# Performance work log

Hardware: AMD Instinct MI355X
Metric: run time of the kernel (lower is better)

Reference implementation:

```python
import jax, jax.numpy as jnp
import numpy as np

D_MODEL = 1024
H = 16
D_K = D_MODEL // H
B, S = 2, 2048
NEG = -1e9


def setup_inputs() -> dict:
    key = jax.random.key(0)
    ks = jax.random.split(key, 8)
    scale = 1.0 / np.sqrt(D_MODEL)
    q = jax.random.normal(ks[0], (B, S, D_MODEL), dtype=jnp.float32)
    k = jax.random.normal(ks[1], (B, S, D_MODEL), dtype=jnp.float32)
    v = jax.random.normal(ks[2], (B, S, D_MODEL), dtype=jnp.float32)
    # causal 0/1 mask, broadcastable to [B, h, S, S]
    mask = jnp.tril(jnp.ones((S, S), dtype=jnp.int32))[None, None, :, :]
    w_q = jax.random.normal(ks[3], (D_MODEL, D_MODEL), dtype=jnp.float32) * scale
    w_k = jax.random.normal(ks[4], (D_MODEL, D_MODEL), dtype=jnp.float32) * scale
    w_v = jax.random.normal(ks[5], (D_MODEL, D_MODEL), dtype=jnp.float32) * scale
    w_o = jax.random.normal(ks[6], (D_MODEL, D_MODEL), dtype=jnp.float32) * scale
    return {"q": q, "k": k, "v": v, "mask": mask,
            "w_q": w_q, "w_k": w_k, "w_v": w_v, "w_o": w_o}


def reference(q, k, v, mask, w_q, w_k, w_v, w_o):
    # projections (no bias)
    def split_heads(x):
        Bn, Sn, _ = x.shape
        return x.reshape(Bn, Sn, H, D_K).transpose(0, 2, 1, 3)  # [B,h,S,d_k]

    qh = split_heads(q @ w_q)
    kh = split_heads(k @ w_k)
    vh = split_heads(v @ w_v)

    scores = jnp.einsum('bhqd,bhkd->bhqk', qh, kh) / jnp.sqrt(
        jnp.asarray(D_K, dtype=qh.dtype))
    scores = jnp.where(mask == 0, jnp.asarray(NEG, dtype=scores.dtype), scores)
    attn = jax.nn.softmax(scores, axis=-1)  # dropout rate 0.0 -> identity
    x = jnp.einsum('bhqk,bhkd->bhqd', attn, vh)  # [B,h,S,d_k]
    x = x.transpose(0, 2, 1, 3).reshape(q.shape[0], q.shape[1], D_MODEL)
    return x @ w_o
```

## Files before the change

### kernel.cpp

```cpp
#include <hip/hip_runtime.h>

#define D_MODEL 1024
#define NH 16
#define DK 64
#define BB 2
#define SS 2048
#define M_TOT (BB*SS)

typedef float f32x4 __attribute__((ext_vector_type(4)));
typedef float f32x16 __attribute__((ext_vector_type(16)));
typedef __bf16 bf16x8 __attribute__((ext_vector_type(8)));
typedef unsigned int u32;

#define QSCALE 0.1803368801f
#define DEFER_THR 11.5416f

__device__ __forceinline__ unsigned short f2bf(float f){
  unsigned int u = __float_as_uint(f);
  unsigned int r = (u + 0x7fffu + ((u >> 16) & 1u)) >> 16;
  return (unsigned short)r;
}

__device__ __forceinline__ void gload_lds16(const void* g, void* l){
  __builtin_amdgcn_global_load_lds((const __attribute__((address_space(1))) void*)g,
                                   (__attribute__((address_space(3))) void*)l,
                                   16, 0, 0);
}

__device__ __forceinline__ void swap_half(u32 a, u32 b, int hi, u32& x, u32& y){
#if __has_builtin(__builtin_amdgcn_permlane32_swap)
  typedef unsigned int uint2v __attribute__((ext_vector_type(2)));
  uint2v r = __builtin_amdgcn_permlane32_swap(a, b, false, false);
  x = r.x; y = r.y;
#else
  u32 as = __shfl_xor(a, 32);
  u32 bs = __shfl_xor(b, 32);
  x = hi ? bs : a;
  y = hi ? b  : as;
#endif
}

__global__ __launch_bounds__(256) void transpose_cvt4(const float* __restrict__ wq,
                                                      const float* __restrict__ wk,
                                                      const float* __restrict__ wv,
                                                      const float* __restrict__ wo,
                                                      unsigned short* __restrict__ WqkvT,
                                                      unsigned short* __restrict__ woT){
  __shared__ float tile[64][65];
  const int which = blockIdx.z;
  const float* w = (which == 0) ? wq : (which == 1) ? wk : (which == 2) ? wv : wo;
  unsigned short* wt = (which == 3) ? woT : (WqkvT + (size_t)which * 1024 * 1024);
  const int N = D_MODEL;
  const int bx = blockIdx.x * 64;
  const int by = blockIdx.y * 64;
  const int t = threadIdx.x;
  #pragma unroll
  for (int i = 0; i < 16; ++i){
    int idx = t + i * 256;
    int r = idx >> 6, c = idx & 63;
    tile[r][c] = w[(size_t)(by + r) * N + bx + c];
  }
  __syncthreads();
  #pragma unroll
  for (int i = 0; i < 16; ++i){
    int idx = t + i * 256;
    int r = idx >> 6, c = idx & 63;
    wt[(size_t)(bx + r) * N + by + c] = f2bf(tile[c][r]);
  }
}

__global__ __launch_bounds__(256) void gemm_qkv(const float* __restrict__ Aq,
                                                const float* __restrict__ Ak,
                                                const float* __restrict__ Av,
                                                const unsigned short* __restrict__ WT,
                                                unsigned short* __restrict__ Qh,
                                                unsigned short* __restrict__ Kh,
                                                unsigned short* __restrict__ VhT){
  __shared__ float          Af[2][128 * 32];
  __shared__ unsigned short Bl[2][128 * 32];
  const int tid = threadIdx.x;
  const int wid = tid >> 6, lane = tid & 63;
  const int lr = lane & 15, lg = lane >> 4;
  const int wm = wid >> 1, wn = wid & 1;
  const int bm = blockIdx.x, bn = blockIdx.y;
  const int seg = bn >> 3;
  const float* A = (seg == 0) ? Aq : (seg == 1) ? Ak : Av;
  const int K = D_MODEL;

  f32x4 acc[4][4];
  #pragma unroll
  for (int i = 0; i < 4; ++i)
    #pragma unroll
    for (int j = 0; j < 4; ++j)
      acc[i][j] = (f32x4){0.f, 0.f, 0.f, 0.f};

  const int lr8 = lane >> 3;
  const int lc8 = lane & 7;
  const int ls8 = lc8 ^ lr8;

  auto stage = [&](int buf, int kt){
    #pragma unroll
    for (int i = 0; i < 4; ++i){
      const int g = wid * 4 + i;
      const int r = g * 8 + lr8;
      gload_lds16(A + (size_t)(bm * 128 + r) * K + kt * 32 + ls8 * 4,
                  &Af[buf][g * 256]);
    }
    #pragma unroll
    for (int rr = 0; rr < 2; ++rr){
      int vt = tid + rr * 256;
      int row = vt >> 2, c8 = (vt & 3) * 8;
      gload_lds16(WT + (size_t)(bn * 128 + row) * K + kt * 32 + c8,
                  &Bl[buf][(wid << 9) + rr * 2048]);
    }
  };

  stage(0, 0);
  int cur = 0;
  for (int kt = 0; kt < 32; ++kt){
    __syncthreads();
    if (kt + 1 < 32) stage(cur ^ 1, kt + 1);
    bf16x8 af[4], bfr[4];
    const int rs = lr & 7;
    #pragma unroll
    for (int i = 0; i < 4; ++i){
      const int row = wm * 64 + i * 16 + lr;
      f32x4 a0 = *(const f32x4*)&Af[cur][row * 32 + (((2 * lg)     ^ rs) * 4)];
      f32x4 a1 = *(const f32x4*)&Af[cur][row * 32 + (((2 * lg + 1) ^ rs) * 4)];
      u32 cc[4];
      asm("v_cvt_pk_bf16_f32 %0, %1, %2" : "=v"(cc[0]) : "v"(a0[0]), "v"(a0[1]));
      asm("v_cvt_pk_bf16_f32 %0, %1, %2" : "=v"(cc[1]) : "v"(a0[2]), "v"(a0[3]));
      asm("v_cvt_pk_bf16_f32 %0, %1, %2" : "=v"(cc[2]) : "v"(a1[0]), "v"(a1[1]));
      asm("v_cvt_pk_bf16_f32 %0, %1, %2" : "=v"(cc[3]) : "v"(a1[2]), "v"(a1[3]));
      __builtin_memcpy(&af[i], cc, 16);
    }
    #pragma unroll
    for (int j = 0; j < 4; ++j)
      bfr[j] = *(const bf16x8*)&Bl[cur][(wn * 64 + j * 16 + lr) * 32 + lg * 8];
    #pragma unroll
    for (int i = 0; i < 4; ++i)
      #pragma unroll
      for (int j = 0; j < 4; ++j)
        acc[i][j] = __builtin_amdgcn_mfma_f32_16x16x32_bf16(af[i], bfr[j], acc[i][j], 0, 0, 0);
    cur ^= 1;
  }

  if (seg < 2){
    unsigned short* O = (seg == 0) ? Qh : Kh;
    const float sc = (seg == 0) ? QSCALE : 1.0f;
    #pragma unroll
    for (int i = 0; i < 4; ++i){
      int row0 = bm * 128 + wm * 64 + i * 16 + lg * 4;
      #pragma unroll
      for (int j = 0; j < 4; ++j){
        int colseg = (bn & 7) * 128 + wn * 64 + j * 16 + lr;
        int h = colseg >> 6, dk = colseg & 63;
        #pragma unroll
        for (int p = 0; p < 4; ++p){
          int rowm = row0 + p;
          int b = rowm >> 11, s = rowm & 2047;
          O[((size_t)(b * NH + h) * SS + s) * DK + dk] = f2bf(acc[i][j][p] * sc);
        }
      }
    }
  } else {
    #pragma unroll
    for (int i = 0; i < 4; ++i){
      int row0 = bm * 128 + wm * 64 + i * 16 + lg * 4;
      int b = row0 >> 11, s = row0 & 2047;
      #pragma unroll
      for (int j = 0; j < 4; ++j){
        int colseg = (bn & 7) * 128 + wn * 64 + j * 16 + lr;
        int h = colseg >> 6, dk = colseg & 63;
        ushort4 o4;
        o4.x = f2bf(acc[i][j][0]); o4.y = f2bf(acc[i][j][1]);
        o4.z = f2bf(acc[i][j][2]); o4.w = f2bf(acc[i][j][3]);
        *(ushort4*)&VhT[((size_t)(b * NH + h) * DK + dk) * SS + s] = o4;
      }
    }
  }
}

__global__ __launch_bounds__(256) void gemm_o64(const unsigned short* __restrict__ A,
                                                const unsigned short* __restrict__ Bt,
                                                float* __restrict__ O){
  __shared__ unsigned short Al[2][64 * 32];
  __shared__ unsigned short Bl[2][128 * 32];
  const int tid = threadIdx.x;
  const int wid = tid >> 6, lane = tid & 63;
  const int lr = lane & 15, lg = lane >> 4;
  const int wm = wid >> 1, wn = wid & 1;
  const int bm = blockIdx.x, bn = blockIdx.y;
  const int K = D_MODEL;

  f32x4 acc[2][4];
  #pragma unroll
  for (int i = 0; i < 2; ++i)
    #pragma unroll
    for (int j = 0; j < 4; ++j)
      acc[i][j] = (f32x4){0.f, 0.f, 0.f, 0.f};

  auto stage = [&](int buf, int kt){
    {
      int row = tid >> 2, c8 = (tid & 3) * 8;
      gload_lds16(A + (size_t)(bm * 64 + row) * K + kt * 32 + c8,
                  &Al[buf][wid << 9]);
    }
    #pragma unroll
    for (int r = 0; r < 2; ++r){
      int vt = tid + r * 256;
      int row = vt >> 2, c8 = (vt & 3) * 8;
      gload_lds16(Bt + (size_t)(bn * 128 + row) * K + kt * 32 + c8,
                  &Bl[buf][(wid << 9) + r * 2048]);
    }
  };

  stage(0, 0);
  int cur = 0;
  for (int kt = 0; kt < 32; ++kt){
    __syncthreads();
    if (kt + 1 < 32) stage(cur ^ 1, kt + 1);
    bf16x8 af[2], bfr[4];
    #pragma unroll
    for (int i = 0; i < 2; ++i)
      af[i] = *(const bf16x8*)&Al[cur][(wm * 32 + i * 16 + lr) * 32 + lg * 8];
    #pragma unroll
    for (int j = 0; j < 4; ++j)
      bfr[j] = *(const bf16x8*)&Bl[cur][(wn * 64 + j * 16 + lr) * 32 + lg * 8];
    #pragma unroll
    for (int i = 0; i < 2; ++i)
      #pragma unroll
      for (int j = 0; j < 4; ++j)
        acc[i][j] = __builtin_amdgcn_mfma_f32_16x16x32_bf16(af[i], bfr[j], acc[i][j], 0, 0, 0);
    cur ^= 1;
  }

  #pragma unroll
  for (int i = 0; i < 2; ++i){
    int row0 = bm * 64 + wm * 32 + i * 16 + lg * 4;
    #pragma unroll
    for (int j = 0; j < 4; ++j){
      int col = bn * 128 + wn * 64 + j * 16 + lr;
      #pragma unroll
      for (int p = 0; p < 4; ++p)
        O[(size_t)(row0 + p) * D_MODEL + col] = acc[i][j][p];
    }
  }
}

__global__ __launch_bounds__(256) void attn_kernel(const unsigned short* __restrict__ Qh,
                                                   const unsigned short* __restrict__ Kh,
                                                   const unsigned short* __restrict__ VhT,
                                                   unsigned short* __restrict__ Oc){
  __shared__ unsigned short SL[2][4][4096];
  const int bh = blockIdx.x;
  const int px = blockIdx.y;
  const int tid = threadIdx.x, wid = tid >> 6, lane = tid & 63;
  const int ln = lane & 31, hi = lane >> 5;
  const int qh = wid & 1, pp = wid >> 1;
  const int b = bh >> 4, h = bh & 15;
  const size_t kvbase = (size_t)bh * SS * DK;

  #pragma unroll 1
  for (int segq = 0; segq < 2; ++segq){
    const int qblk = segq ? (31 - px) : px;
    const int q0 = qblk * 64 + qh * 32;
    const int Tw = 2 * qblk + qh;
    const int R = (qblk + 2) >> 1;

    const unsigned short* qp = Qh + kvbase + (size_t)(q0 + ln) * DK + hi * 8;
    bf16x8 qbv[4];
    #pragma unroll
    for (int c = 0; c < 4; ++c) qbv[c] = *(const bf16x8*)(qp + c * 16);

    f32x16 oa0 = {0,0,0,0,0,0,0,0,0,0,0,0,0,0,0,0};
    f32x16 oa1 = {0,0,0,0,0,0,0,0,0,0,0,0,0,0,0,0};
    float m = -1e30f, ls = 0.f;

    auto stage = [&](int bufb, int r){
      const int k0A = (2 * r) * 64;
      const int k0B = k0A + 64;
      const bool haveB = (2 * r + 1) <= qblk;
      #pragma unroll
      for (int i = 0; i < 2; ++i){
        const int c = i * 256 + tid;
        const int row = c >> 3;
        const int slot = (c & 7) ^ (row & 7);
        const int ldso = (i * 256 + wid * 64) * 8;
        gload_lds16(Kh  + kvbase + (size_t)(k0A + row) * DK + slot * 8, &SL[bufb][0][ldso]);
        gload_lds16(VhT + kvbase + (size_t)row * SS + k0A + slot * 8,   &SL[bufb][1][ldso]);
        if (haveB){
          gload_lds16(Kh  + kvbase + (size_t)(k0B + row) * DK + slot * 8, &SL[bufb][2][ldso]);
          gload_lds16(VhT + kvbase + (size_t)row * SS + k0B + slot * 8,   &SL[bufb][3][ldso]);
        }
      }
    };

    stage(0, 0);
    int cur = 0;
    #pragma unroll 1
    for (int r = 0; r < R; ++r){
      __syncthreads();
      if (r + 1 < R) stage(cur ^ 1, r + 1);

      const int t = 2 * r + pp;
      if (t <= qblk){
        const unsigned short* Kb = SL[cur][pp * 2];
        const unsigned short* Vb = SL[cur][pp * 2 + 1];

        f32x16 sta = {0,0,0,0,0,0,0,0,0,0,0,0,0,0,0,0};
        f32x16 stb = {0,0,0,0,0,0,0,0,0,0,0,0,0,0,0,0};
        __builtin_amdgcn_s_setprio(1);
        #pragma unroll
        for (int c = 0; c < 4; ++c){
          const int po = ((c * 2 + hi) ^ (ln & 7)) * 8;
          bf16x8 kfa = *(const bf16x8*)&Kb[ln * 64 + po];
          bf16x8 kfb = *(const bf16x8*)&Kb[(32 + ln) * 64 + po];
          sta = __builtin_amdgcn_mfma_f32_32x32x16_bf16(kfa, qbv[c], sta, 0, 0, 0);
          stb = __builtin_amdgcn_mfma_f32_32x32x16_bf16(kfb, qbv[c], stb, 0, 0, 0);
        }
        __builtin_amdgcn_s_setprio(0);

        const int ta = 2 * t, tb = 2 * t + 1;
        if (tb == Tw){
          #pragma unroll
          for (int rr = 0; rr < 16; ++rr){
            int kg = (rr & 3) + 8 * (rr >> 2) + 4 * hi;
            if (kg > ln) stb[rr] = -1e30f;
          }
        } else if (ta == Tw){
          #pragma unroll
          for (int rr = 0; rr < 16; ++rr){
            int kg = (rr & 3) + 8 * (rr >> 2) + 4 * hi;
            if (kg > ln) sta[rr] = -1e30f;
            stb[rr] = -1e30f;
          }
        }

        float tm[8];
        #pragma unroll
        for (int i = 0; i < 8; ++i)
          tm[i] = fmaxf(fmaxf(sta[2*i], sta[2*i+1]), fmaxf(stb[2*i], stb[2*i+1]));
        float mx = fmaxf(fmaxf(fmaxf(tm[0], tm[1]), fmaxf(tm[2], tm[3])),
                         fmaxf(fmaxf(tm[4], tm[5]), fmaxf(tm[6], tm[7])));
        mx = fmaxf(mx, __shfl_xor(mx, 32));

        if (__any(mx > m + DEFER_THR)){
          const float mn = fmaxf(m, mx);
          const float fac = __builtin_amdgcn_exp2f(m - mn);
          m = mn;
          ls *= fac;
          #pragma unroll
          for (int rr = 0; rr < 16; ++rr){ oa0[rr] *= fac; oa1[rr] *= fac; }
        }

        #pragma unroll
        for (int rr = 0; rr < 16; ++rr){
          sta[rr] = __builtin_amdgcn_exp2f(sta[rr] - m);
          stb[rr] = __builtin_amdgcn_exp2f(stb[rr] - m);
        }
        float sm[8];
        #pragma unroll
        for (int i = 0; i < 8; ++i)
          sm[i] = (sta[2*i] + sta[2*i+1]) + (stb[2*i] + stb[2*i+1]);
        float rsum = ((sm[0] + sm[1]) + (sm[2] + sm[3])) + ((sm[4] + sm[5]) + (sm[6] + sm[7]));
        rsum += __shfl_xor(rsum, 32);
        ls += rsum;

        u32 ca[8], cb[8];
        #pragma unroll
        for (int i = 0; i < 8; ++i){
          asm("v_cvt_pk_bf16_f32 %0, %1, %2" : "=v"(ca[i]) : "v"(sta[2*i]), "v"(sta[2*i+1]));
          asm("v_cvt_pk_bf16_f32 %0, %1, %2" : "=v"(cb[i]) : "v"(stb[2*i]), "v"(stb[2*i+1]));
        }
        u32 w0[4], w1[4], w2[4], w3[4];
        swap_half(ca[0], ca[2], hi, w0[0], w0[2]);
        swap_half(ca[1], ca[3], hi, w0[1], w0[3]);
        swap_half(ca[4], ca[6], hi, w1[0], w1[2]);
        swap_half(ca[5], ca[7], hi, w1[1], w1[3]);
        swap_half(cb[0], cb[2], hi, w2[0], w2[2]);
        swap_half(cb[1], cb[3], hi, w2[1], w2[3]);
        swap_half(cb[4], cb[6], hi, w3[0], w3[2]);
        swap_half(cb[5], cb[7], hi, w3[1], w3[3]);
        bf16x8 pf[4];
        __builtin_memcpy(&pf[0], w0, 16);
        __builtin_memcpy(&pf[1], w1, 16);
        __builtin_memcpy(&pf[2], w2, 16);
        __builtin_memcpy(&pf[3], w3, 16);

        __builtin_amdgcn_s_setprio(1);
        #pragma unroll
        for (int ks = 0; ks < 4; ++ks){
          const int po = ((ks * 2 + hi) ^ (ln & 7)) * 8;
          bf16x8 v0 = *(const bf16x8*)&Vb[ln * 64 + po];
          bf16x8 v1 = *(const bf16x8*)&Vb[(32 + ln) * 64 + po];
          oa0 = __builtin_amdgcn_mfma_f32_32x32x16_bf16(v0, pf[ks], oa0, 0, 0, 0);
          oa1 = __builtin_amdgcn_mfma_f32_32x32x16_bf16(v1, pf[ks], oa1, 0, 0, 0);
        }
        __builtin_amdgcn_s_setprio(0);
      }
      cur ^= 1;
    }
    __syncthreads();

    float* oL  = (float*)&SL[0][0][0];
    float* mLs = (float*)&SL[0][2][0];
    if (wid >= 2){
      const int w = wid - 2;
      #pragma unroll
      for (int rr = 0; rr < 16; ++rr){
        oL[(w * 32 + rr) * 64 + lane]      = oa0[rr];
        oL[(w * 32 + 16 + rr) * 64 + lane] = oa1[rr];
      }
      if (hi == 0){ mLs[w * 32 + ln] = m; mLs[64 + w * 32 + ln] = ls; }
    }
    __syncthreads();
    if (wid < 2){
      const float m1  = mLs[wid * 32 + ln];
      const float ls1 = mLs[64 + wid * 32 + ln];
      const float mstar = fmaxf(m, m1);
      const float f0 = __builtin_amdgcn_exp2f(m  - mstar);
      const float f1 = __builtin_amdgcn_exp2f(m1 - mstar);
      const float inv = 1.0f / (f0 * ls + f1 * ls1);
      const size_t rowbase = ((size_t)b * SS + q0 + ln) * D_MODEL + h * DK;
      #pragma unroll
      for (int g = 0; g < 4; ++g){
        ushort4 o4;
        o4.x = f2bf((f0 * oa0[4*g + 0] + f1 * oL[(wid * 32 + 4*g + 0) * 64 + lane]) * inv);
        o4.y = f2bf((f0 * oa0[4*g + 1] + f1 * oL[(wid * 32 + 4*g + 1) * 64 + lane]) * inv);
        o4.z = f2bf((f0 * oa0[4*g + 2] + f1 * oL[(wid * 32 + 4*g + 2) * 64 + lane]) * inv);
        o4.w = f2bf((f0 * oa0[4*g + 3] + f1 * oL[(wid * 32 + 4*g + 3) * 64 + lane]) * inv);
        *(ushort4*)&Oc[rowbase + 8*g + 4*hi] = o4;
      }
      #pragma unroll
      for (int g = 0; g < 4; ++g){
        ushort4 o4;
        o4.x = f2bf((f0 * oa1[4*g + 0] + f1 * oL[(wid * 32 + 16 + 4*g + 0) * 64 + lane]) * inv);
        o4.y = f2bf((f0 * oa1[4*g + 1] + f1 * oL[(wid * 32 + 16 + 4*g + 1) * 64 + lane]) * inv);
        o4.z = f2bf((f0 * oa1[4*g + 2] + f1 * oL[(wid * 32 + 16 + 4*g + 2) * 64 + lane]) * inv);
        o4.w = f2bf((f0 * oa1[4*g + 3] + f1 * oL[(wid * 32 + 16 + 4*g + 3) * 64 + lane]) * inv);
        *(ushort4*)&Oc[rowbase + 32 + 8*g + 4*hi] = o4;
      }
    }
    __syncthreads();
  }
}

extern "C" void kernel_launch(void* const* d_in, const int* in_sizes, int n_in,
                              void* d_out, int out_size, void* d_ws, size_t ws_size,
                              hipStream_t stream){
  const float* q  = (const float*)d_in[0];
  const float* k  = (const float*)d_in[1];
  const float* v  = (const float*)d_in[2];
  const float* wq = (const float*)d_in[4];
  const float* wk = (const float*)d_in[5];
  const float* wv = (const float*)d_in[6];
  const float* wo = (const float*)d_in[7];
  float* out = (float*)d_out;

  char* ws = (char*)d_ws;
  const size_t MB = 1024 * 1024;
  unsigned short* WqkvT  = (unsigned short*)(ws + 0 * MB);
  unsigned short* woT    = (unsigned short*)(ws + 6 * MB);
  unsigned short* Qh     = (unsigned short*)(ws + 8 * MB);
  unsigned short* Kh     = (unsigned short*)(ws + 16 * MB);
  unsigned short* VhT    = (unsigned short*)(ws + 24 * MB);
  unsigned short* attnb  = (unsigned short*)(ws + 32 * MB);

  dim3 tg(16, 16, 4);
  transpose_cvt4<<<tg, 256, 0, stream>>>(wq, wk, wv, wo, WqkvT, woT);

  dim3 gqkv(M_TOT / 128, 3 * D_MODEL / 128);
  gemm_qkv<<<gqkv, 256, 0, stream>>>(q, k, v, WqkvT, Qh, Kh, VhT);

  dim3 ga(BB * NH, SS / 128);
  attn_kernel<<<ga, 256, 0, stream>>>(Qh, Kh, VhT, attnb);

  dim3 go(M_TOT / 64, D_MODEL / 128);
  gemm_o64<<<go, 256, 0, stream>>>(attnb, woT, out);
}
```

Before: 118.7 us.

## Convert QKV GEMM A tile to bf16 in registers before LDS store

The QKV projection GEMM used to stream fp32 activations straight into LDS with direct global-to-LDS loads, then convert to bf16 on every fragment read. It now loads the fp32 A tile into registers, converts once to bf16, and writes it to a bf16 LDS buffer after the MFMA block. This halves LDS footprint and read traffic for A and avoids converting the same data repeatedly across warps. In exchange it loses the async direct-to-LDS path, adds register pressure, and drops the XOR swizzle, which may bring LDS bank conflicts.

```diff
diff --git a/kernel.cpp b/kernel.cpp
--- a/kernel.cpp
+++ b/kernel.cpp
@@ -76,7 +76,7 @@
                                                 unsigned short* __restrict__ Qh,
                                                 unsigned short* __restrict__ Kh,
                                                 unsigned short* __restrict__ VhT){
-  __shared__ float          Af[2][128 * 32];
+  __shared__ unsigned short Al[2][128 * 32];
   __shared__ unsigned short Bl[2][128 * 32];
   const int tid = threadIdx.x;
   const int wid = tid >> 6, lane = tid & 63;
@@ -94,18 +94,27 @@
     for (int j = 0; j < 4; ++j)
       acc[i][j] = (f32x4){0.f, 0.f, 0.f, 0.f};
 
-  const int lr8 = lane >> 3;
-  const int lc8 = lane & 7;
-  const int ls8 = lc8 ^ lr8;
-
-  auto stage = [&](int buf, int kt){
-    #pragma unroll
-    for (int i = 0; i < 4; ++i){
-      const int g = wid * 4 + i;
-      const int r = g * 8 + lr8;
-      gload_lds16(A + (size_t)(bm * 128 + r) * K + kt * 32 + ls8 * 4,
-                  &Af[buf][g * 256]);
-    }
+  const int arow  = tid >> 3;
+  const int aslot = tid & 7;
+
+  f32x4 ar[4];
+
+  auto loadA = [&](int kt){
+    #pragma unroll
+    for (int p = 0; p < 4; ++p)
+      ar[p] = *(const f32x4*)&A[(size_t)(bm * 128 + p * 32 + arow) * K + kt * 32 + aslot * 4];
+  };
+  auto writeA = [&](int buf){
+    #pragma unroll
+    for (int p = 0; p < 4; ++p){
+      u32 c0, c1;
+      asm("v_cvt_pk_bf16_f32 %0, %1, %2" : "=v"(c0) : "v"(ar[p][0]), "v"(ar[p][1]));
+      asm("v_cvt_pk_bf16_f32 %0, %1, %2" : "=v"(c1) : "v"(ar[p][2]), "v"(ar[p][3]));
+      uint2 wv2 = {c0, c1};
+      *(uint2*)&Al[buf][(p * 32 + arow) * 32 + aslot * 4] = wv2;
+    }
+  };
+  auto stageB = [&](int buf, int kt){
     #pragma unroll
     for (int rr = 0; rr < 2; ++rr){
       int vt = tid + rr * 256;
@@ -115,25 +124,21 @@
     }
   };
 
-  stage(0, 0);
+  loadA(0);
+  stageB(0, 0);
+  writeA(0);
+
   int cur = 0;
   for (int kt = 0; kt < 32; ++kt){
     __syncthreads();
-    if (kt + 1 < 32) stage(cur ^ 1, kt + 1);
+    if (kt + 1 < 32){
+      loadA(kt + 1);
+      stageB(cur ^ 1, kt + 1);
+    }
     bf16x8 af[4], bfr[4];
-    const int rs = lr & 7;
-    #pragma unroll
-    for (int i = 0; i < 4; ++i){
-      const int row = wm * 64 + i * 16 + lr;
-      f32x4 a0 = *(const f32x4*)&Af[cur][row * 32 + (((2 * lg)     ^ rs) * 4)];
-      f32x4 a1 = *(const f32x4*)&Af[cur][row * 32 + (((2 * lg + 1) ^ rs) * 4)];
-      u32 cc[4];
-      asm("v_cvt_pk_bf16_f32 %0, %1, %2" : "=v"(cc[0]) : "v"(a0[0]), "v"(a0[1]));
-      asm("v_cvt_pk_bf16_f32 %0, %1, %2" : "=v"(cc[1]) : "v"(a0[2]), "v"(a0[3]));
-      asm("v_cvt_pk_bf16_f32 %0, %1, %2" : "=v"(cc[2]) : "v"(a1[0]), "v"(a1[1]));
-      asm("v_cvt_pk_bf16_f32 %0, %1, %2" : "=v"(cc[3]) : "v"(a1[2]), "v"(a1[3]));
-      __builtin_memcpy(&af[i], cc, 16);
-    }
+    #pragma unroll
+    for (int i = 0; i < 4; ++i)
+      af[i] = *(const bf16x8*)&Al[cur][(wm * 64 + i * 16 + lr) * 32 + lg * 8];
     #pragma unroll
     for (int j = 0; j < 4; ++j)
       bfr[j] = *(const bf16x8*)&Bl[cur][(wn * 64 + j * 16 + lr) * 32 + lg * 8];
@@ -142,6 +147,7 @@
       #pragma unroll
       for (int j = 0; j < 4; ++j)
         acc[i][j] = __builtin_amdgcn_mfma_f32_16x16x32_bf16(af[i], bfr[j], acc[i][j], 0, 0, 0);
+    if (kt + 1 < 32) writeA(cur ^ 1);
     cur ^= 1;
   }
 
```

Result: faster. 114.5 us (-3.6%).
